# Kernel optimization log

Hardware: AMD Instinct MI355X
Metric: run time of the kernel (lower is better)

The kernel has to match this reference:

```python
import jax, jax.numpy as jnp
import numpy as np

IMAGE = 128            # canvas_size == image_size -> resize is identity
N_LINES = 32
N_SEGMENTS = 2
N_POINTS = 5           # control points per line (2 shared-endpoint quadratic beziers)
N_COLOR = 3
COORDPAIRS = np.array([[0, 1, 2], [2, 3, 4]])  # (n_segments, 3)
N_SAMPLES = 10         # polyline samples for bezier edt2 (explicit 10 in source)
POWER = 2.0            # power at progress=0 (= config.power_i)
SIGMA2 = 0.05          # annealed sigma2 at progress=0
EPS = 1e-10
BS = 4


def setup_inputs() -> dict:
    key = jax.random.key(0)
    k1, k2, k3, k4 = jax.random.split(key, 4)
    position = 0.5 * jax.random.normal(k1, (BS, N_LINES, N_POINTS * 2), jnp.float32)
    radius = jax.random.uniform(k2, (BS, N_LINES, 1), jnp.float32, minval=0.3, maxval=1.0)
    color = jax.random.uniform(k3, (BS, N_LINES, N_COLOR), jnp.float32)
    background = jax.random.uniform(k4, (BS, N_COLOR), jnp.float32)
    return {"position": position, "radius": radius, "color": color, "background": background}


def _render(position, radius, color, background):
    bs = position.shape[0]
    r = jnp.linspace(-1.0, 1.0, IMAGE)
    gy, gx = jnp.meshgrid(r, r, indexing="ij")
    grid = jnp.stack([gy, gx], axis=-1)                      # (H, W, 2)

    # --- reshape_params (background='keep', n_back=0) ---
    lines = position.reshape(bs, N_LINES, N_POINTS, 2)
    segs = lines[:, :, COORDPAIRS]                           # (bs, nl, nseg, 3, 2)
    # smooth bezier: reflect control point of segments after the first
    segs = segs.at[:, :, 1:, 1].set(2.0 * segs[:, :, 1:, 0] - segs[:, :, 1:, 1])
    curves = segs.reshape(bs, N_LINES * N_SEGMENTS, 3, 2)    # (bs, N, 3, 2)

    sigma = (radius ** 2).reshape(bs, N_LINES, 1, 1)
    sigma = jnp.repeat(sigma, N_SEGMENTS, axis=1) * SIGMA2   # (bs, N, 1, 1)
    col = jnp.repeat(color, N_SEGMENTS, axis=1)[:, :, :, None, None]  # (bs, N, nc, 1, 1)

    # --- curve_edt2_polyline: sample quadratic bezier, min segment distance ---
    t = jnp.linspace(0.0, 1.0, N_SAMPLES)
    w = jnp.stack([(1.0 - t) ** 2, 2.0 * t * (1.0 - t), t ** 2], axis=0)  # (3, T)
    pts = jnp.einsum("bnkc,kt->bntc", curves, w)             # (bs, N, T, 2)
    a, b = pts[:, :, :-1], pts[:, :, 1:]                     # (bs, N, S=T-1, 2)
    v = b - a
    v_ = v[:, :, :, None, None, :]
    d = grid[None, None, None] - a[:, :, :, None, None, :]   # (bs, N, S, H, W, 2)
    vv = jnp.sum(v * v, axis=-1)[:, :, :, None, None]
    tp = jnp.clip(jnp.sum(d * v_, axis=-1) / (vv + EPS), 0.0, 1.0)
    diff = d - tp[..., None] * v_
    edt2 = jnp.min(jnp.sum(diff * diff, axis=-1), axis=2)    # (bs, N, H, W)

    # --- intensity + rasterize + over-composite ---
    intensity = jnp.exp(-((edt2 / sigma) ** POWER))          # (bs, N, H, W)
    rasters = col * intensity[:, :, None]                    # (bs, N, nc, H, W)
    canvas = jnp.broadcast_to(background[:, None, :, None, None],
                              (bs, 1, N_COLOR, IMAGE, IMAGE))
    rasters = jnp.concatenate([rasters, canvas], axis=1)     # (bs, N+1, nc, H, W)
    inten_c = jnp.broadcast_to(intensity[:, :, None],
                               (bs, intensity.shape[1], N_COLOR, IMAGE, IMAGE))
    inten_all = jnp.concatenate([inten_c, jnp.ones_like(canvas)], axis=1)
    linv = 1.0 - inten_all + EPS
    # 'over' composite front-to-back along stroke dim: exclusive cumprod weights
    w_excl = jnp.concatenate([jnp.ones_like(linv[:, :1]),
                              jnp.cumprod(linv, axis=1)[:, :-1]], axis=1)
    images = jnp.sum(rasters * w_excl, axis=1)               # (bs, nc, H, W)
    return jnp.clip(images, 0.0, 1.0)


def reference(position, radius, color, background):
    return _render(position, radius, color, background)
```

## Files before the change

### kernel.cpp

```cpp
#include <hip/hip_runtime.h>

#define IMAGE   128
#define NLINES  32
#define NCURVE  64
#define NSUB    9
#define PIX     (IMAGE*IMAGE)
#define BS      4
#define NCHUNK  8
#define CPC     8
#define PPL     4

__global__ __launch_bounds__(512, 2)
void render_kernel(const float* __restrict__ pos,
                   const float* __restrict__ rad,
                   const float* __restrict__ col,
                   const float* __restrict__ bg,
                   float* __restrict__ out)
{
    __shared__ float4 s_sub4[NCURVE*NSUB];
    __shared__ float2 s_sub2[NCURVE*NSUB];
    __shared__ float4 s_cur[NCURVE];
    __shared__ float4 s_part[NCHUNK*256];

    const int tid  = threadIdx.x;
    const int b    = blockIdx.x >> 6;
    const int tile = blockIdx.x & 63;

    for (int e = tid; e < NCURVE*NSUB; e += 512) {
        const int n    = e / NSUB;
        const int j    = e - n*NSUB;
        const int line = n >> 1;
        const int seg  = n & 1;
        const float* P = pos + (b*NLINES + line)*10;
        float c0x, c0y, c1x, c1y, c2x, c2y;
        if (seg == 0) {
            c0x = P[0]; c0y = P[1];
            c1x = P[2]; c1y = P[3];
            c2x = P[4]; c2y = P[5];
        } else {
            const float q2x = P[4], q2y = P[5];
            const float q3x = P[6], q3y = P[7];
            c0x = q2x;             c0y = q2y;
            c1x = 2.0f*q2x - q3x;  c1y = 2.0f*q2y - q3y;
            c2x = P[8];            c2y = P[9];
        }
        const float t0 = (float)j     * (1.0f/9.0f);
        const float t1 = (float)(j+1) * (1.0f/9.0f);
        float ax, ay, bx, by;
        {
            const float mt = 1.0f - t0;
            const float w0 = mt*mt, w1 = 2.0f*t0*mt, w2 = t0*t0;
            ax = w0*c0x + w1*c1x + w2*c2x;
            ay = w0*c0y + w1*c1y + w2*c2y;
        }
        {
            const float mt = 1.0f - t1;
            const float w0 = mt*mt, w1 = 2.0f*t1*mt, w2 = t1*t1;
            bx = w0*c0x + w1*c1x + w2*c2x;
            by = w0*c0y + w1*c1y + w2*c2y;
        }
        const float vx = bx - ax, vy = by - ay;
        const float rvv = 1.0f / (vx*vx + vy*vy + 1e-10f);
        s_sub4[e] = make_float4(ax, ay, vx, vy);
        s_sub2[e] = make_float2(vx*rvv, vy*rvv);
    }
    if (tid < NCURVE) {
        const int line = tid >> 1;
        const float r  = rad[b*NLINES + line];
        s_cur[tid] = make_float4(1.0f / (r*r*0.05f),
                                 col[(b*NLINES + line)*3 + 0],
                                 col[(b*NLINES + line)*3 + 1],
                                 col[(b*NLINES + line)*3 + 2]);
    }
    __syncthreads();

    const int lane  = tid & 63;
    const int chunk = tid >> 6;

    float g0[PPL], g1[PPL];
    float aR[PPL], aG[PPL], aB[PPL], T[PPL];
    #pragma unroll
    for (int k = 0; k < PPL; ++k) {
        const int p = tile*256 + k*64 + lane;
        g0[k] = -1.0f + (float)(p >> 7)  * (2.0f/127.0f);
        g1[k] = -1.0f + (float)(p & 127) * (2.0f/127.0f);
        aR[k] = 0.0f; aG[k] = 0.0f; aB[k] = 0.0f; T[k] = 1.0f;
    }

    for (int i = 0; i < CPC; ++i) {
        const int n = chunk*CPC + i;
        float edt2[PPL];
        #pragma unroll
        for (int k = 0; k < PPL; ++k) edt2[k] = 3.4e38f;
        #pragma unroll 3
        for (int j = 0; j < NSUB; ++j) {
            const float4 s = s_sub4[n*NSUB + j];
            const float2 w = s_sub2[n*NSUB + j];
            #pragma unroll
            for (int k = 0; k < PPL; ++k) {
                const float d0 = g0[k] - s.x;
                const float d1 = g1[k] - s.y;
                const float tp = fminf(fmaxf(d0*w.x + d1*w.y, 0.0f), 1.0f);
                const float e0 = fmaf(-tp, s.z, d0);
                const float e1 = fmaf(-tp, s.w, d1);
                edt2[k] = fminf(edt2[k], fmaf(e0, e0, e1*e1));
            }
        }
        const float4 cu = s_cur[n];
        #pragma unroll
        for (int k = 0; k < PPL; ++k) {
            const float xs = edt2[k] * cu.x;
            const float I  = __expf(-xs*xs);
            const float wI = I * T[k];
            aR[k] = fmaf(cu.y, wI, aR[k]);
            aG[k] = fmaf(cu.z, wI, aG[k]);
            aB[k] = fmaf(cu.w, wI, aB[k]);
            T[k] *= (1.0f - I + 1e-10f);
        }
    }
    #pragma unroll
    for (int k = 0; k < PPL; ++k)
        s_part[chunk*256 + k*64 + lane] = make_float4(aR[k], aG[k], aB[k], T[k]);
    __syncthreads();

    if (tid < 256) {
        float4 acc = s_part[tid];
        float C0 = acc.x, C1 = acc.y, C2 = acc.z, Tt = acc.w;
        #pragma unroll
        for (int c = 1; c < NCHUNK; ++c) {
            const float4 q = s_part[c*256 + tid];
            C0 = fmaf(Tt, q.x, C0);
            C1 = fmaf(Tt, q.y, C1);
            C2 = fmaf(Tt, q.z, C2);
            Tt *= q.w;
        }
        C0 = fmaf(Tt, bg[b*3+0], C0);
        C1 = fmaf(Tt, bg[b*3+1], C1);
        C2 = fmaf(Tt, bg[b*3+2], C2);
        const int po = tile*256 + tid;
        out[(b*3+0)*PIX + po] = fminf(fmaxf(C0, 0.0f), 1.0f);
        out[(b*3+1)*PIX + po] = fminf(fmaxf(C1, 0.0f), 1.0f);
        out[(b*3+2)*PIX + po] = fminf(fmaxf(C2, 0.0f), 1.0f);
    }
}

extern "C" void kernel_launch(void* const* d_in, const int* in_sizes, int n_in,
                              void* d_out, int out_size, void* d_ws, size_t ws_size,
                              hipStream_t stream) {
    const float* pos = (const float*)d_in[0];
    const float* rad = (const float*)d_in[1];
    const float* col = (const float*)d_in[2];
    const float* bg  = (const float*)d_in[3];
    float* out = (float*)d_out;

    render_kernel<<<dim3(BS*64), dim3(512), 0, stream>>>(pos, rad, col, bg, out);
}
```

Baseline: 68.92 us.

## Cull curves per two-row tile by bounding box and use exp2 intensity

Each block covers two image rows, so the kernel now computes a y-extent bounding box per curve, padded by a radius-dependent margin. It builds a compacted list of the curves that can affect those rows using a wave ballot. Only active curves are split across the eight chunks, which skips distance work for curves far from the tile while keeping front-to-back order. It also folds the log2(e) factor into the sigma constant so it can use a hardware exp2, clamps with fmed3, shares per-row deltas, and drops the epsilon in the transmittance update. Culled curves are treated as having zero intensity, a tiny approximation, and chunk load can become unbalanced.

Measured after the change: 67.68 us. No clear change (-1.8%).

```diff
diff --git a/kernel.cpp b/kernel.cpp
--- a/kernel.cpp
+++ b/kernel.cpp
@@ -7,8 +7,12 @@
 #define PIX     (IMAGE*IMAGE)
 #define BS      4
 #define NCHUNK  8
-#define CPC     8
-#define PPL     4
+
+#if __has_builtin(__builtin_amdgcn_exp2f)
+#define EXP2F(x) __builtin_amdgcn_exp2f(x)
+#else
+#define EXP2F(x) exp2f(x)
+#endif
 
 __global__ __launch_bounds__(512, 2)
 void render_kernel(const float* __restrict__ pos,
@@ -20,11 +24,16 @@
     __shared__ float4 s_sub4[NCURVE*NSUB];
     __shared__ float2 s_sub2[NCURVE*NSUB];
     __shared__ float4 s_cur[NCURVE];
+    __shared__ int    s_active[NCURVE];
+    __shared__ unsigned long long s_mask;
     __shared__ float4 s_part[NCHUNK*256];
 
     const int tid  = threadIdx.x;
     const int b    = blockIdx.x >> 6;
     const int tile = blockIdx.x & 63;
+
+    const float yb0 = -1.0f + (float)(tile*2) * (2.0f/127.0f);
+    const float yb1 = yb0 + (2.0f/127.0f);
 
     for (int e = tid; e < NCURVE*NSUB; e += 512) {
         const int n    = e / NSUB;
@@ -32,94 +41,115 @@
         const int line = n >> 1;
         const int seg  = n & 1;
         const float* P = pos + (b*NLINES + line)*10;
-        float c0x, c0y, c1x, c1y, c2x, c2y;
+        float c0a, c0b, c1a, c1b, c2a, c2b;
         if (seg == 0) {
-            c0x = P[0]; c0y = P[1];
-            c1x = P[2]; c1y = P[3];
-            c2x = P[4]; c2y = P[5];
+            c0a = P[0]; c0b = P[1];
+            c1a = P[2]; c1b = P[3];
+            c2a = P[4]; c2b = P[5];
         } else {
-            const float q2x = P[4], q2y = P[5];
-            const float q3x = P[6], q3y = P[7];
-            c0x = q2x;             c0y = q2y;
-            c1x = 2.0f*q2x - q3x;  c1y = 2.0f*q2y - q3y;
-            c2x = P[8];            c2y = P[9];
+            const float q2a = P[4], q2b = P[5];
+            const float q3a = P[6], q3b = P[7];
+            c0a = q2a;             c0b = q2b;
+            c1a = 2.0f*q2a - q3a;  c1b = 2.0f*q2b - q3b;
+            c2a = P[8];            c2b = P[9];
         }
         const float t0 = (float)j     * (1.0f/9.0f);
         const float t1 = (float)(j+1) * (1.0f/9.0f);
-        float ax, ay, bx, by;
+        float aa, ab, ba, bb;
         {
             const float mt = 1.0f - t0;
             const float w0 = mt*mt, w1 = 2.0f*t0*mt, w2 = t0*t0;
-            ax = w0*c0x + w1*c1x + w2*c2x;
-            ay = w0*c0y + w1*c1y + w2*c2y;
+            aa = w0*c0a + w1*c1a + w2*c2a;
+            ab = w0*c0b + w1*c1b + w2*c2b;
         }
         {
             const float mt = 1.0f - t1;
             const float w0 = mt*mt, w1 = 2.0f*t1*mt, w2 = t1*t1;
-            bx = w0*c0x + w1*c1x + w2*c2x;
-            by = w0*c0y + w1*c1y + w2*c2y;
+            ba = w0*c0a + w1*c1a + w2*c2a;
+            bb = w0*c0b + w1*c1b + w2*c2b;
         }
-        const float vx = bx - ax, vy = by - ay;
-        const float rvv = 1.0f / (vx*vx + vy*vy + 1e-10f);
-        s_sub4[e] = make_float4(ax, ay, vx, vy);
-        s_sub2[e] = make_float2(vx*rvv, vy*rvv);
+        const float v0 = ba - aa, v1 = bb - ab;
+        const float rvv = 1.0f / (v0*v0 + v1*v1 + 1e-10f);
+        s_sub4[e] = make_float4(aa, ab, v0, v1);
+        s_sub2[e] = make_float2(v0*rvv, v1*rvv);
     }
-    if (tid < NCURVE) {
-        const int line = tid >> 1;
-        const float r  = rad[b*NLINES + line];
-        s_cur[tid] = make_float4(1.0f / (r*r*0.05f),
-                                 col[(b*NLINES + line)*3 + 0],
-                                 col[(b*NLINES + line)*3 + 1],
-                                 col[(b*NLINES + line)*3 + 2]);
+    if (tid >= 448) {
+        const int n    = tid - 448;
+        const int line = n >> 1;
+        const int seg  = n & 1;
+        const float* P = pos + (b*NLINES + line)*10;
+        float a0, a1, a2;
+        if (seg == 0) { a0 = P[0]; a1 = P[2];             a2 = P[4]; }
+        else          { a0 = P[4]; a1 = 2.0f*P[4] - P[6]; a2 = P[8]; }
+        const float r = rad[b*NLINES + line];
+        const float m = 0.45f * r;
+        const float lo = fminf(a0, fminf(a1, a2)) - m;
+        const float hi = fmaxf(a0, fmaxf(a1, a2)) + m;
+        const bool act = (lo <= yb1) && (hi >= yb0);
+        const unsigned long long mask = __ballot(act);
+        const int lane = tid & 63;
+        const int rank = __popcll(mask & ((1ull << lane) - 1ull));
+        if (act) s_active[rank] = n;
+        if (lane == 0) s_mask = mask;
+        s_cur[n] = make_float4(1.2011224087864498f / (r*r*0.05f),
+                               col[(b*NLINES + line)*3 + 0],
+                               col[(b*NLINES + line)*3 + 1],
+                               col[(b*NLINES + line)*3 + 2]);
     }
     __syncthreads();
 
     const int lane  = tid & 63;
     const int chunk = tid >> 6;
+    const int A     = __popcll(s_mask);
+    const int start = (chunk * A) >> 3;
+    const int end   = ((chunk + 1) * A) >> 3;
 
-    float g0[PPL], g1[PPL];
-    float aR[PPL], aG[PPL], aB[PPL], T[PPL];
+    const float x0 = -1.0f + (float)lane        * (2.0f/127.0f);
+    const float x1 = -1.0f + (float)(lane + 64) * (2.0f/127.0f);
+
+    float aR[4], aG[4], aB[4], T[4];
     #pragma unroll
-    for (int k = 0; k < PPL; ++k) {
-        const int p = tile*256 + k*64 + lane;
-        g0[k] = -1.0f + (float)(p >> 7)  * (2.0f/127.0f);
-        g1[k] = -1.0f + (float)(p & 127) * (2.0f/127.0f);
-        aR[k] = 0.0f; aG[k] = 0.0f; aB[k] = 0.0f; T[k] = 1.0f;
-    }
+    for (int k = 0; k < 4; ++k) { aR[k] = 0.0f; aG[k] = 0.0f; aB[k] = 0.0f; T[k] = 1.0f; }
 
-    for (int i = 0; i < CPC; ++i) {
-        const int n = chunk*CPC + i;
-        float edt2[PPL];
+    #pragma unroll 1
+    for (int ii = start; ii < end; ++ii) {
+        const int n    = s_active[ii];
+        const int base = n*NSUB;
+        float edt2[4];
         #pragma unroll
-        for (int k = 0; k < PPL; ++k) edt2[k] = 3.4e38f;
-        #pragma unroll 3
+        for (int k = 0; k < 4; ++k) edt2[k] = 3.4e38f;
+        #pragma unroll
         for (int j = 0; j < NSUB; ++j) {
-            const float4 s = s_sub4[n*NSUB + j];
-            const float2 w = s_sub2[n*NSUB + j];
+            const float4 s = s_sub4[base + j];
+            const float2 w = s_sub2[base + j];
+            const float dY0 = yb0 - s.x;
+            const float dY1 = yb1 - s.x;
+            const float dX0 = x0  - s.y;
+            const float dX1 = x1  - s.y;
             #pragma unroll
-            for (int k = 0; k < PPL; ++k) {
-                const float d0 = g0[k] - s.x;
-                const float d1 = g1[k] - s.y;
-                const float tp = fminf(fmaxf(d0*w.x + d1*w.y, 0.0f), 1.0f);
-                const float e0 = fmaf(-tp, s.z, d0);
-                const float e1 = fmaf(-tp, s.w, d1);
+            for (int k = 0; k < 4; ++k) {
+                const float dA = (k & 2) ? dY1 : dY0;
+                const float dB = (k & 1) ? dX1 : dX0;
+                const float tp = __builtin_amdgcn_fmed3f(fmaf(dB, w.y, dA*w.x), 0.0f, 1.0f);
+                const float e0 = fmaf(-tp, s.z, dA);
+                const float e1 = fmaf(-tp, s.w, dB);
                 edt2[k] = fminf(edt2[k], fmaf(e0, e0, e1*e1));
             }
         }
         const float4 cu = s_cur[n];
         #pragma unroll
-        for (int k = 0; k < PPL; ++k) {
+        for (int k = 0; k < 4; ++k) {
             const float xs = edt2[k] * cu.x;
-            const float I  = __expf(-xs*xs);
+            const float I  = EXP2F(-(xs*xs));
             const float wI = I * T[k];
             aR[k] = fmaf(cu.y, wI, aR[k]);
             aG[k] = fmaf(cu.z, wI, aG[k]);
             aB[k] = fmaf(cu.w, wI, aB[k]);
-            T[k] *= (1.0f - I + 1e-10f);
+            T[k] *= (1.0f - I);
         }
     }
     #pragma unroll
-    for (int k = 0; k < PPL; ++k)
+    for (int k = 0; k < 4; ++k)
         s_part[chunk*256 + k*64 + lane] = make_float4(aR[k], aG[k], aB[k], T[k]);
     __syncthreads();
 
```
